# Optimization experiments

Measured on AMD Instinct MI355X. Metric: run time of the kernel, lower is better.

Reference implementation:

```python
import jax, jax.numpy as jnp
import numpy as np

B, J, E = 4096, 32, 256

def setup_inputs() -> dict:
    key = jax.random.key(0)
    ks = jax.random.split(key, 7)
    return {
        "x": jax.random.normal(ks[0], (B, E), dtype=jnp.float32),
        "state": jax.random.normal(ks[1], (B, J * E), dtype=jnp.float32),
        "keys": jax.random.normal(ks[2], (J, E), dtype=jnp.float32) * 0.1,
        "U": jax.random.normal(ks[3], (E, E), dtype=jnp.float32) * 0.1,
        "V": jax.random.normal(ks[4], (E, E), dtype=jnp.float32) * 0.1,
        "W": jax.random.normal(ks[5], (E, E), dtype=jnp.float32) * 0.1,
        "bias": jax.random.normal(ks[6], (E,), dtype=jnp.float32) * 0.1,
    }

def reference(x, state, keys, U, V, W, bias):
    b, je = state.shape
    j = keys.shape[0]
    e = x.shape[1]
    s = state.reshape(b, j, e)                      # [B,J,E]
    # gate_j = sigmoid(<x, state_j> + <x, key_j>)
    gate = jax.nn.sigmoid(jnp.einsum('be,bje->bj', x, s)
                          + x @ keys.T)             # [B,J]
    # candidate_j = relu(U s_j + bias + W x + V k_j)
    cand = jax.nn.relu(jnp.einsum('bje,fe->bjf', s, U)
                       + bias
                       + (x @ W.T)[:, None, :]
                       + (keys @ V.T)[None, :, :])  # [B,J,E]
    s_next = s + gate[..., None] * cand
    norm = jnp.abs(jnp.linalg.norm(s_next, axis=-1, keepdims=True)) + 1e-8
    s_next = s_next / norm
    return s_next.reshape(b, je)
```

## Files before the change

kernel.cpp:

```cpp
#include <hip/hip_runtime.h>
#include <hip/hip_bf16.h>

typedef __bf16 bf16_t;
typedef __attribute__((ext_vector_type(8))) __bf16 bf16x8;
typedef __attribute__((ext_vector_type(4))) float f32x4;

#define E_DIM 256
#define J_DIM 32
#define B_DIM 4096
#define M_DIM (B_DIM * J_DIM)
#define BM 128
#define BK 32
#define LDA 40
#define LDB 40
#define LDAF 33

#define XK_LDA (E_DIM + 4)

__device__ inline bf16x8 cvt8(const float* __restrict__ p) {
    f32x4 a = *(const f32x4*)p;
    f32x4 b = *(const f32x4*)(p + 4);
    bf16x8 r;
    r[0] = (bf16_t)a[0]; r[1] = (bf16_t)a[1]; r[2] = (bf16_t)a[2]; r[3] = (bf16_t)a[3];
    r[4] = (bf16_t)b[0]; r[5] = (bf16_t)b[1]; r[6] = (bf16_t)b[2]; r[7] = (bf16_t)b[3];
    return r;
}

__global__ __launch_bounds__(256) void xkvkb_kernel(
    const float* __restrict__ x, const float* __restrict__ keys,
    const float* __restrict__ V, const float* __restrict__ bias,
    float* __restrict__ xk, float* __restrict__ vkb) {
    __shared__ float smem[(J_DIM + 8) * XK_LDA];
    int tid = threadIdx.x, bid = blockIdx.x;
    if (bid < 512) {
        float* sK = smem;
        float* sX = smem + J_DIM * XK_LDA;
        int b0 = bid * 8;
#pragma unroll
        for (int it = 0; it < 8; ++it) {
            int t = it * 256 + tid;
            int r = t >> 6, c = (t & 63) * 4;
            *(f32x4*)(sK + r * XK_LDA + c) = *(const f32x4*)(keys + (size_t)r * E_DIM + c);
        }
#pragma unroll
        for (int it = 0; it < 2; ++it) {
            int t = it * 256 + tid;
            int r = t >> 6, c = (t & 63) * 4;
            *(f32x4*)(sX + r * XK_LDA + c) =
                *(const f32x4*)(x + (size_t)b0 * E_DIM + (size_t)r * E_DIM + c);
        }
        __syncthreads();
        int j = tid & 31, bl = tid >> 5;
        float acc = 0.f;
        for (int e = 0; e < E_DIM; e += 4) {
            f32x4 xv = *(const f32x4*)(sX + bl * XK_LDA + e);
            f32x4 kv = *(const f32x4*)(sK + j * XK_LDA + e);
#pragma unroll
            for (int i = 0; i < 4; ++i) acc += xv[i] * kv[i];
        }
        xk[(size_t)(b0 + bl) * J_DIM + j] = acc;
    } else {
        int j = bid - 512, f = tid;
        float* sk = smem;
        sk[f] = keys[(size_t)j * E_DIM + f];
        __syncthreads();
        float acc = bias[f];
        for (int e = 0; e < E_DIM; e += 4) {
            f32x4 vv = *(const f32x4*)(V + (size_t)f * E_DIM + e);
#pragma unroll
            for (int i = 0; i < 4; ++i) acc += vv[i] * sk[e + i];
        }
        vkb[(size_t)j * E_DIM + f] = acc;
    }
}

__global__ __launch_bounds__(256) void wx_kernel(const float* __restrict__ x,
                                                 const float* __restrict__ W,
                                                 float* __restrict__ wx) {
    __shared__ __align__(16) bf16_t sA[64][LDA];
    __shared__ __align__(16) bf16_t sBw[64][LDB];
    int tid = threadIdx.x;
    int w = tid >> 6, lane = tid & 63, quad = lane >> 4, l15 = lane & 15;
    int m0 = (blockIdx.x >> 2) * 64, n0 = (blockIdx.x & 3) * 64;
    f32x4 acc[4];
#pragma unroll
    for (int nt = 0; nt < 4; ++nt)
#pragma unroll
        for (int r = 0; r < 4; ++r) acc[nt][r] = 0.f;
    int arow = tid >> 2, akk = (tid & 3) * 8;
    for (int kc = 0; kc < 8; ++kc) {
        int k0 = kc * BK;
        __syncthreads();
        *(bf16x8*)(&sA[arow][akk]) = cvt8(x + (size_t)(m0 + arow) * E_DIM + k0 + akk);
        *(bf16x8*)(&sBw[arow][akk]) = cvt8(W + (size_t)(n0 + arow) * E_DIM + k0 + akk);
        __syncthreads();
        bf16x8 af = *(const bf16x8*)(&sA[w * 16 + l15][quad * 8]);
#pragma unroll
        for (int nt = 0; nt < 4; ++nt) {
            bf16x8 bfr = *(const bf16x8*)(&sBw[nt * 16 + l15][quad * 8]);
            acc[nt] = __builtin_amdgcn_mfma_f32_16x16x32_bf16(af, bfr, acc[nt], 0, 0, 0);
        }
    }
#pragma unroll
    for (int nt = 0; nt < 4; ++nt)
#pragma unroll
        for (int r = 0; r < 4; ++r)
            wx[(size_t)(m0 + w * 16 + quad * 4 + r) * E_DIM + n0 + nt * 16 + l15] =
                acc[nt][r];
}

__global__ __launch_bounds__(512) void memcell_kernel(
    const float* __restrict__ x, const float* __restrict__ state,
    const float* __restrict__ U, const float* __restrict__ wx,
    const float* __restrict__ xk, const float* __restrict__ vkb,
    float* __restrict__ out) {
    __shared__ __align__(16) bf16_t sA[BM][LDA];
    __shared__ __align__(16) bf16_t sB[E_DIM][LDB];
    __shared__ __align__(16) float sAf[BM][LDAF];
    __shared__ __align__(16) float sXf[4][E_DIM];
    int tid = threadIdx.x;
    int w = tid >> 6, lane = tid & 63, quad = lane >> 4, l15 = lane & 15;
    int m0 = blockIdx.x * BM;
    int b0 = m0 >> 5;
    f32x4 acc[16];
#pragma unroll
    for (int nt = 0; nt < 16; ++nt)
#pragma unroll
        for (int r = 0; r < 4; ++r) acc[nt][r] = 0.f;
    float gdot = 0.f;
    if (tid < 128) {
        int bb = tid >> 5, p = tid & 31;
        f32x4 xa = *(const f32x4*)(x + (size_t)(b0 + bb) * E_DIM + p * 8);
        f32x4 xb = *(const f32x4*)(x + (size_t)(b0 + bb) * E_DIM + p * 8 + 4);
        *(f32x4*)(&sXf[bb][p * 8]) = xa;
        *(f32x4*)(&sXf[bb][p * 8 + 4]) = xb;
    }
    int arow = tid >> 2, akk = (tid & 3) * 8;
    for (int kc = 0; kc < 8; ++kc) {
        int k0 = kc * BK;
        __syncthreads();
        {
            const float* sp = state + (size_t)(m0 + arow) * E_DIM + k0 + akk;
            f32x4 a = *(const f32x4*)sp;
            f32x4 b = *(const f32x4*)(sp + 4);
            *(f32x4*)(&sAf[arow][akk]) = a;
            *(f32x4*)(&sAf[arow][akk + 4]) = b;
            bf16x8 r;
            r[0] = (bf16_t)a[0]; r[1] = (bf16_t)a[1]; r[2] = (bf16_t)a[2]; r[3] = (bf16_t)a[3];
            r[4] = (bf16_t)b[0]; r[5] = (bf16_t)b[1]; r[6] = (bf16_t)b[2]; r[7] = (bf16_t)b[3];
            *(bf16x8*)(&sA[arow][akk]) = r;
        }
#pragma unroll
        for (int it = 0; it < 2; ++it) {
            int t = it * 512 + tid;
            int n = t >> 2, kk = (t & 3) * 8;
            *(bf16x8*)(&sB[n][kk]) = cvt8(U + (size_t)n * E_DIM + k0 + kk);
        }
        __syncthreads();
        bf16x8 af = *(const bf16x8*)(&sA[w * 16 + l15][quad * 8]);
#pragma unroll
        for (int i = 0; i < 8; ++i)
            gdot += sAf[w * 16 + l15][quad * 8 + i] * sXf[w >> 1][k0 + quad * 8 + i];
#pragma unroll
        for (int nt = 0; nt < 16; ++nt) {
            bf16x8 bfr = *(const bf16x8*)(&sB[nt * 16 + l15][quad * 8]);
            acc[nt] = __builtin_amdgcn_mfma_f32_16x16x32_bf16(af, bfr, acc[nt], 0, 0, 0);
        }
    }
    gdot += __shfl_xor(gdot, 16);
    gdot += __shfl_xor(gdot, 32);
    int bw = b0 + (w >> 1);
    float garg = gdot + xk[(size_t)bw * J_DIM + (w & 1) * 16 + l15];
    float gv = 1.f / (1.f + expf(-garg));
    float gate[4];
#pragma unroll
    for (int r = 0; r < 4; ++r) gate[r] = __shfl(gv, quad * 4 + r);
    float sumsq[4] = {0.f, 0.f, 0.f, 0.f};
    const float* wxrow = wx + (size_t)bw * E_DIM;
#pragma unroll
    for (int nt = 0; nt < 16; ++nt) {
        int f = nt * 16 + l15;
        float wxf = wxrow[f];
#pragma unroll
        for (int r = 0; r < 4; ++r) {
            int rl = quad * 4 + r;
            int jidx = (w & 1) * 16 + rl;
            float c = acc[nt][r] + wxf + vkb[(size_t)jidx * E_DIM + f];
            c = fmaxf(c, 0.f);
            float sv = state[(size_t)(m0 + w * 16 + rl) * E_DIM + f];
            float t = fmaf(gate[r], c, sv);
            acc[nt][r] = t;
            sumsq[r] += t * t;
        }
    }
    float rn[4];
#pragma unroll
    for (int r = 0; r < 4; ++r) {
        float s2 = sumsq[r];
        s2 += __shfl_xor(s2, 1);
        s2 += __shfl_xor(s2, 2);
        s2 += __shfl_xor(s2, 4);
        s2 += __shfl_xor(s2, 8);
        rn[r] = 1.f / (sqrtf(s2) + 1e-8f);
    }
#pragma unroll
    for (int nt = 0; nt < 16; ++nt)
#pragma unroll
        for (int r = 0; r < 4; ++r)
            out[(size_t)(m0 + w * 16 + quad * 4 + r) * E_DIM + nt * 16 + l15] =
                acc[nt][r] * rn[r];
}

extern "C" void kernel_launch(void* const* d_in, const int* in_sizes, int n_in,
                              void* d_out, int out_size, void* d_ws, size_t ws_size,
                              hipStream_t stream) {
    const float* x     = (const float*)d_in[0];
    const float* state = (const float*)d_in[1];
    const float* keys  = (const float*)d_in[2];
    const float* U     = (const float*)d_in[3];
    const float* V     = (const float*)d_in[4];
    const float* W     = (const float*)d_in[5];
    const float* bias  = (const float*)d_in[6];
    float* out = (float*)d_out;

    float* wsf = (float*)d_ws;
    float* wx  = wsf;
    float* xk  = wsf + (size_t)B_DIM * E_DIM;
    float* vkb = xk + (size_t)B_DIM * J_DIM;

    xkvkb_kernel<<<544, 256, 0, stream>>>(x, keys, V, bias, xk, vkb);
    wx_kernel<<<256, 256, 0, stream>>>(x, W, wx);
    memcell_kernel<<<M_DIM / BM, 512, 0, stream>>>(x, state, U, wx, xk, vkb, out);
}
```

Measured before the change: 360.0 us.

## Keep full U resident in LDS and loop blocks over four M tiles

The main kernel now converts all of U to bf16 once per block into LDS and keeps it there. Each block handles four 128-row tiles instead of one, and the grid shrinks by four. State rows are loaded straight from global into registers as MFMA A fragments, and the gate dot product is formed there, removing the per-K-chunk LDS staging and barriers. The trade-offs are about 135KB of LDS per block, which allows only one block per CU, 256 blocks to cover the whole GPU, and uncoalesced-ish per-lane global loads of state.

```diff
diff --git a/kernel.cpp b/kernel.cpp
--- a/kernel.cpp
+++ b/kernel.cpp
@@ -9,11 +9,10 @@
 #define J_DIM 32
 #define B_DIM 4096
 #define M_DIM (B_DIM * J_DIM)
-#define BM 128
 #define BK 32
 #define LDA 40
 #define LDB 40
-#define LDAF 33
+#define LDU 264
 
 #define XK_LDA (E_DIM + 4)
 
@@ -114,101 +113,91 @@
     const float* __restrict__ U, const float* __restrict__ wx,
     const float* __restrict__ xk, const float* __restrict__ vkb,
     float* __restrict__ out) {
-    __shared__ __align__(16) bf16_t sA[BM][LDA];
-    __shared__ __align__(16) bf16_t sB[E_DIM][LDB];
-    __shared__ __align__(16) float sAf[BM][LDAF];
-    __shared__ __align__(16) float sXf[4][E_DIM];
+    __shared__ __align__(16) bf16_t sU[E_DIM][LDU];
     int tid = threadIdx.x;
     int w = tid >> 6, lane = tid & 63, quad = lane >> 4, l15 = lane & 15;
-    int m0 = blockIdx.x * BM;
-    int b0 = m0 >> 5;
-    f32x4 acc[16];
-#pragma unroll
-    for (int nt = 0; nt < 16; ++nt)
-#pragma unroll
-        for (int r = 0; r < 4; ++r) acc[nt][r] = 0.f;
-    float gdot = 0.f;
-    if (tid < 128) {
-        int bb = tid >> 5, p = tid & 31;
-        f32x4 xa = *(const f32x4*)(x + (size_t)(b0 + bb) * E_DIM + p * 8);
-        f32x4 xb = *(const f32x4*)(x + (size_t)(b0 + bb) * E_DIM + p * 8 + 4);
-        *(f32x4*)(&sXf[bb][p * 8]) = xa;
-        *(f32x4*)(&sXf[bb][p * 8 + 4]) = xb;
-    }
-    int arow = tid >> 2, akk = (tid & 3) * 8;
-    for (int kc = 0; kc < 8; ++kc) {
-        int k0 = kc * BK;
-        __syncthreads();
-        {
-            const float* sp = state + (size_t)(m0 + arow) * E_DIM + k0 + akk;
-            f32x4 a = *(const f32x4*)sp;
-            f32x4 b = *(const f32x4*)(sp + 4);
-            *(f32x4*)(&sAf[arow][akk]) = a;
-            *(f32x4*)(&sAf[arow][akk + 4]) = b;
-            bf16x8 r;
-            r[0] = (bf16_t)a[0]; r[1] = (bf16_t)a[1]; r[2] = (bf16_t)a[2]; r[3] = (bf16_t)a[3];
-            r[4] = (bf16_t)b[0]; r[5] = (bf16_t)b[1]; r[6] = (bf16_t)b[2]; r[7] = (bf16_t)b[3];
-            *(bf16x8*)(&sA[arow][akk]) = r;
-        }
-#pragma unroll
-        for (int it = 0; it < 2; ++it) {
-            int t = it * 512 + tid;
-            int n = t >> 2, kk = (t & 3) * 8;
-            *(bf16x8*)(&sB[n][kk]) = cvt8(U + (size_t)n * E_DIM + k0 + kk);
-        }
-        __syncthreads();
-        bf16x8 af = *(const bf16x8*)(&sA[w * 16 + l15][quad * 8]);
-#pragma unroll
-        for (int i = 0; i < 8; ++i)
-            gdot += sAf[w * 16 + l15][quad * 8 + i] * sXf[w >> 1][k0 + quad * 8 + i];
+
+#pragma unroll
+    for (int it = 0; it < 16; ++it) {
+        int s = it * 512 + tid;
+        int n = s >> 5, kk = (s & 31) * 8;
+        *(bf16x8*)(&sU[n][kk]) = cvt8(U + (size_t)n * E_DIM + kk);
+    }
+    __syncthreads();
+
+    int mbase = blockIdx.x * 512;
+    for (int mt = 0; mt < 4; ++mt) {
+        int m0 = mbase + mt * 128;
+        int bw = (m0 >> 5) + (w >> 1);
+        const float* sp = state + (size_t)(m0 + w * 16 + l15) * E_DIM + quad * 8;
+        const float* xp = x + (size_t)bw * E_DIM + quad * 8;
+        f32x4 acc[16];
+#pragma unroll
+        for (int nt = 0; nt < 16; ++nt)
+#pragma unroll
+            for (int r = 0; r < 4; ++r) acc[nt][r] = 0.f;
+        float gdot = 0.f;
+        for (int kc = 0; kc < 8; ++kc) {
+            int k0 = kc * BK;
+            f32x4 a0  = *(const f32x4*)(sp + k0);
+            f32x4 a1  = *(const f32x4*)(sp + k0 + 4);
+            f32x4 xv0 = *(const f32x4*)(xp + k0);
+            f32x4 xv1 = *(const f32x4*)(xp + k0 + 4);
+            bf16x8 af;
+#pragma unroll
+            for (int i = 0; i < 4; ++i) { af[i] = (bf16_t)a0[i]; af[4 + i] = (bf16_t)a1[i]; }
+#pragma unroll
+            for (int i = 0; i < 4; ++i) gdot += a0[i] * xv0[i];
+#pragma unroll
+            for (int i = 0; i < 4; ++i) gdot += a1[i] * xv1[i];
+#pragma unroll
+            for (int nt = 0; nt < 16; ++nt) {
+                bf16x8 bfr = *(const bf16x8*)(&sU[nt * 16 + l15][k0 + quad * 8]);
+                acc[nt] = __builtin_amdgcn_mfma_f32_16x16x32_bf16(af, bfr, acc[nt], 0, 0, 0);
+            }
+        }
+        gdot += __shfl_xor(gdot, 16);
+        gdot += __shfl_xor(gdot, 32);
+        float garg = gdot + xk[(size_t)bw * J_DIM + (w & 1) * 16 + l15];
+        float gv = 1.f / (1.f + expf(-garg));
+        float gate[4];
+#pragma unroll
+        for (int r = 0; r < 4; ++r) gate[r] = __shfl(gv, quad * 4 + r);
+        float sumsq[4] = {0.f, 0.f, 0.f, 0.f};
+        const float* wxrow = wx + (size_t)bw * E_DIM;
 #pragma unroll
         for (int nt = 0; nt < 16; ++nt) {
-            bf16x8 bfr = *(const bf16x8*)(&sB[nt * 16 + l15][quad * 8]);
-            acc[nt] = __builtin_amdgcn_mfma_f32_16x16x32_bf16(af, bfr, acc[nt], 0, 0, 0);
-        }
-    }
-    gdot += __shfl_xor(gdot, 16);
-    gdot += __shfl_xor(gdot, 32);
-    int bw = b0 + (w >> 1);
-    float garg = gdot + xk[(size_t)bw * J_DIM + (w & 1) * 16 + l15];
-    float gv = 1.f / (1.f + expf(-garg));
-    float gate[4];
-#pragma unroll
-    for (int r = 0; r < 4; ++r) gate[r] = __shfl(gv, quad * 4 + r);
-    float sumsq[4] = {0.f, 0.f, 0.f, 0.f};
-    const float* wxrow = wx + (size_t)bw * E_DIM;
-#pragma unroll
-    for (int nt = 0; nt < 16; ++nt) {
-        int f = nt * 16 + l15;
-        float wxf = wxrow[f];
+            int f = nt * 16 + l15;
+            float wxf = wxrow[f];
+#pragma unroll
+            for (int r = 0; r < 4; ++r) {
+                int rl = quad * 4 + r;
+                int jidx = (w & 1) * 16 + rl;
+                float c = acc[nt][r] + wxf + vkb[(size_t)jidx * E_DIM + f];
+                c = fmaxf(c, 0.f);
+                float sv = state[(size_t)(m0 + w * 16 + rl) * E_DIM + f];
+                float t = fmaf(gate[r], c, sv);
+                acc[nt][r] = t;
+                sumsq[r] += t * t;
+            }
+        }
+        float rn[4];
 #pragma unroll
         for (int r = 0; r < 4; ++r) {
-            int rl = quad * 4 + r;
-            int jidx = (w & 1) * 16 + rl;
-            float c = acc[nt][r] + wxf + vkb[(size_t)jidx * E_DIM + f];
-            c = fmaxf(c, 0.f);
-            float sv = state[(size_t)(m0 + w * 16 + rl) * E_DIM + f];
-            float t = fmaf(gate[r], c, sv);
-            acc[nt][r] = t;
-            sumsq[r] += t * t;
-        }
-    }
-    float rn[4];
-#pragma unroll
-    for (int r = 0; r < 4; ++r) {
-        float s2 = sumsq[r];
-        s2 += __shfl_xor(s2, 1);
-        s2 += __shfl_xor(s2, 2);
-        s2 += __shfl_xor(s2, 4);
-        s2 += __shfl_xor(s2, 8);
-        rn[r] = 1.f / (sqrtf(s2) + 1e-8f);
-    }
-#pragma unroll
-    for (int nt = 0; nt < 16; ++nt)
-#pragma unroll
-        for (int r = 0; r < 4; ++r)
-            out[(size_t)(m0 + w * 16 + quad * 4 + r) * E_DIM + nt * 16 + l15] =
-                acc[nt][r] * rn[r];
+            float s2 = sumsq[r];
+            s2 += __shfl_xor(s2, 1);
+            s2 += __shfl_xor(s2, 2);
+            s2 += __shfl_xor(s2, 4);
+            s2 += __shfl_xor(s2, 8);
+            rn[r] = 1.f / (sqrtf(s2) + 1e-8f);
+        }
+#pragma unroll
+        for (int nt = 0; nt < 16; ++nt)
+#pragma unroll
+            for (int r = 0; r < 4; ++r)
+                out[(size_t)(m0 + w * 16 + quad * 4 + r) * E_DIM + nt * 16 + l15] =
+                    acc[nt][r] * rn[r];
+    }
 }
 
 extern "C" void kernel_launch(void* const* d_in, const int* in_sizes, int n_in,
@@ -230,5 +219,5 @@
 
     xkvkb_kernel<<<544, 256, 0, stream>>>(x, keys, V, bias, xk, vkb);
     wx_kernel<<<256, 256, 0, stream>>>(x, W, wx);
-    memcell_kernel<<<M_DIM / BM, 512, 0, stream>>>(x, state, U, wx, xk, vkb, out);
-}
+    memcell_kernel<<<M_DIM / 512, 512, 0, stream>>>(x, state, U, wx, xk, vkb, out);
+}
```

Result: slower. 693.0 us (+92.5%).
